# Kernel tuning notes

Measured on AMD Instinct MI355X. Metric: run time of the kernel, lower is better.

The kernel has to match this reference:

```python
import jax, jax.numpy as jnp
import numpy as np

HIDDEN, N_HEADS, N_KV, HEAD_DIM, CACHE_LEN = 4096, 32, 8, 128, 4096
N_REP = N_HEADS // N_KV
BATCH = 32


def setup_inputs() -> dict:
    key = jax.random.key(0)
    ks = jax.random.split(key, 7)
    x = jax.random.normal(ks[0], (BATCH, 1, HIDDEN), jnp.float32)
    k_cache = jax.random.normal(ks[1], (BATCH, N_KV, CACHE_LEN, HEAD_DIM), jnp.float32)
    v_cache = jax.random.normal(ks[2], (BATCH, N_KV, CACHE_LEN, HEAD_DIM), jnp.float32)
    s = 1.0 / np.sqrt(HIDDEN)
    wq = jax.random.normal(ks[3], (HIDDEN, N_HEADS * HEAD_DIM), jnp.float32) * s
    wk = jax.random.normal(ks[4], (HIDDEN, N_KV * HEAD_DIM), jnp.float32) * s
    wv = jax.random.normal(ks[5], (HIDDEN, N_KV * HEAD_DIM), jnp.float32) * s
    wo = jax.random.normal(ks[6], (N_HEADS * HEAD_DIM, HIDDEN), jnp.float32) * s
    return {"x": x, "k_cache": k_cache, "v_cache": v_cache,
            "wq": wq, "wk": wk, "wv": wv, "wo": wo}


def reference(x, k_cache, v_cache, wq, wk, wv, wo):
    b = x.shape[0]
    xt = x[:, 0, :]  # (b, hidden) -- single decode token
    # Projections; group query heads by kv head: (b, n_kv, n_rep, d)
    q = (xt @ wq).reshape(b, N_KV, N_REP, HEAD_DIM)
    k_new = (xt @ wk).reshape(b, N_KV, HEAD_DIM)
    v_new = (xt @ wv).reshape(b, N_KV, HEAD_DIM)
    scale = 1.0 / np.sqrt(HEAD_DIM).astype(np.float32)
    # GQA attention over cache: scores (b, n_kv, n_rep, cache_len)
    cache_scores = jnp.einsum('bknd,bksd->bkns', q, k_cache) * scale
    cache_probs = jax.nn.softmax(cache_scores, axis=-1)
    cache_out = jnp.einsum('bkns,bksd->bknd', cache_probs, v_cache)
    # New-token term: softmax over a length-1 axis is identically 1,
    # so the separate-pass attention over the new K/V reduces to v_new
    # broadcast over the n_rep query heads (keeps wk/wv in the graph via v_new).
    new_out = jnp.broadcast_to(v_new[:, :, None, :], cache_out.shape)
    out = (cache_out + new_out).reshape(b, 1, N_HEADS * HEAD_DIM)
    return out @ wo
```

## Files before the change

### kernel.cpp

```cpp
#include <hip/hip_runtime.h>
#include <hip/hip_bf16.h>

#define HIDDEN   4096
#define N_HEADS  32
#define N_KV     8
#define N_REP    4
#define HEAD_DIM 128
#define CACHE    4096
#define BATCH    32

#define PJ_THREADS 128
#define PJ_COLS    256
#define PJ_HCHUNK  128

typedef float f4v __attribute__((ext_vector_type(4)));

__global__ __launch_bounds__(128) void proj_kernel(
    const float* __restrict__ X,
    const float* __restrict__ W1, int ld1, int ncol1,
    const float* __restrict__ W2, int ld2,
    float* __restrict__ part, int ncols)
{
    __shared__ float xs[32 * PJ_HCHUNK];
    const int hc   = blockIdx.y;
    const int h0   = hc * PJ_HCHUNK;
    const int col0 = blockIdx.x * PJ_COLS;
    const int tid  = threadIdx.x;

    for (int i = tid * 4; i < 32 * PJ_HCHUNK; i += PJ_THREADS * 4) {
        int b = i >> 7, j = i & 127;
        *(float4*)&xs[i] = *(const float4*)&X[(size_t)b * HIDDEN + h0 + j];
    }
    __syncthreads();

    const int col = col0 + tid * 2;
    const float* Wp;
    size_t ld;
    if (col < ncol1) { Wp = W1 + (size_t)h0 * ld1 + col;           ld = ld1; }
    else             { Wp = W2 + (size_t)h0 * ld2 + (col - ncol1); ld = ld2; }

    float2 acc[32];
#pragma unroll
    for (int b = 0; b < 32; ++b) acc[b] = make_float2(0.f, 0.f);

    float2 wc[8], wn[8];
#pragma unroll
    for (int r = 0; r < 8; ++r) wc[r] = *(const float2*)(Wp + r * ld);
    Wp += 8 * ld;

#define PJ_COMPUTE(XR)                                                  \
    _Pragma("unroll")                                                   \
    for (int b = 0; b < 32; ++b) {                                      \
        float4 x0 = *(const float4*)((XR) + b * PJ_HCHUNK);             \
        float4 x1 = *(const float4*)((XR) + b * PJ_HCHUNK + 4);         \
        acc[b].x = fmaf(x0.x, wc[0].x, acc[b].x);                       \
        acc[b].y = fmaf(x0.x, wc[0].y, acc[b].y);                       \
        acc[b].x = fmaf(x0.y, wc[1].x, acc[b].x);                       \
        acc[b].y = fmaf(x0.y, wc[1].y, acc[b].y);                       \
        acc[b].x = fmaf(x0.z, wc[2].x, acc[b].x);                       \
        acc[b].y = fmaf(x0.z, wc[2].y, acc[b].y);                       \
        acc[b].x = fmaf(x0.w, wc[3].x, acc[b].x);                       \
        acc[b].y = fmaf(x0.w, wc[3].y, acc[b].y);                       \
        acc[b].x = fmaf(x1.x, wc[4].x, acc[b].x);                       \
        acc[b].y = fmaf(x1.x, wc[4].y, acc[b].y);                       \
        acc[b].x = fmaf(x1.y, wc[5].x, acc[b].x);                       \
        acc[b].y = fmaf(x1.y, wc[5].y, acc[b].y);                       \
        acc[b].x = fmaf(x1.z, wc[6].x, acc[b].x);                       \
        acc[b].y = fmaf(x1.z, wc[6].y, acc[b].y);                       \
        acc[b].x = fmaf(x1.w, wc[7].x, acc[b].x);                       \
        acc[b].y = fmaf(x1.w, wc[7].y, acc[b].y);                       \
    }

    for (int bt = 0; bt < (PJ_HCHUNK / 8) - 1; ++bt) {
#pragma unroll
        for (int r = 0; r < 8; ++r) wn[r] = *(const float2*)(Wp + r * ld);
        const float* xr = xs + bt * 8;
        PJ_COMPUTE(xr)
#pragma unroll
        for (int r = 0; r < 8; ++r) wc[r] = wn[r];
        Wp += 8 * ld;
    }
    {
        const float* xr = xs + PJ_HCHUNK - 8;
        PJ_COMPUTE(xr)
    }
#undef PJ_COMPUTE

    float* dst = part + ((size_t)hc * 32) * ncols + col;
#pragma unroll
    for (int b = 0; b < 32; ++b)
        *(float2*)(dst + (size_t)b * ncols) = acc[b];
}

__global__ __launch_bounds__(256) void combine_proj(
    const float* __restrict__ part, int ncols,
    float* __restrict__ dst1, int ld1, int ncol1,
    float* __restrict__ dst2, int ld2)
{
    const int col = blockIdx.x * 256 + threadIdx.x;
    const int b   = blockIdx.y;
    float s = 0.f;
#pragma unroll
    for (int i = 0; i < 32; ++i) s += part[((size_t)i * 32 + b) * ncols + col];
    if (col < ncol1) dst1[(size_t)b * ld1 + col] = s;
    else             dst2[(size_t)b * ld2 + (col - ncol1)] = s;
}


template<int CTRL>
__device__ __forceinline__ float dpp_ror(float x) {
    return __int_as_float(__builtin_amdgcn_update_dpp(
        0, __float_as_int(x), CTRL, 0xF, 0xF, true));
}

#define DOT8(PART, QA, QB)                         \
    PART = QA.x * ka.x;                            \
    PART = fmaf(QA.y, ka.y, PART);                 \
    PART = fmaf(QA.z, ka.z, PART);                 \
    PART = fmaf(QA.w, ka.w, PART);                 \
    PART = fmaf(QB.x, kb4.x, PART);                \
    PART = fmaf(QB.y, kb4.y, PART);                \
    PART = fmaf(QB.z, kb4.z, PART);                \
    PART = fmaf(QB.w, kb4.w, PART);

#define RED4_DPP(CTRL)                             \
    part0 += dpp_ror<CTRL>(part0);                 \
    part1 += dpp_ror<CTRL>(part1);                 \
    part2 += dpp_ror<CTRL>(part2);                 \
    part3 += dpp_ror<CTRL>(part3);

#define PVROW(PR, OA, OB)                          \
    OA.x = fmaf(PR, va.x,  OA.x);                  \
    OA.y = fmaf(PR, va.y,  OA.y);                  \
    OA.z = fmaf(PR, va.z,  OA.z);                  \
    OA.w = fmaf(PR, va.w,  OA.w);                  \
    OB.x = fmaf(PR, vb4.x, OB.x);                  \
    OB.y = fmaf(PR, vb4.y, OB.y);                  \
    OB.z = fmaf(PR, vb4.z, OB.z);                  \
    OB.w = fmaf(PR, vb4.w, OB.w);

#define REDV(V, M)                                 \
    V.x += __shfl_xor(V.x, M, 64);                 \
    V.y += __shfl_xor(V.y, M, 64);                 \
    V.z += __shfl_xor(V.z, M, 64);                 \
    V.w += __shfl_xor(V.w, M, 64);

__global__ __launch_bounds__(256, 4) void attn_kernel(
    const float* __restrict__ q,
    const float* __restrict__ kc,
    const float* __restrict__ vc,
    float* __restrict__ po,
    float* __restrict__ pl)
{
    const int bid   = blockIdx.x;
    const int pair  = bid >> 3;
    const int sg    = bid & 7;
    const int tid   = threadIdx.x;
    const int w     = tid >> 6;
    const int lane  = tid & 63;
    const int g     = lane >> 4;
    const int l     = lane & 15;
    const int split = sg * 4 + w;
    const int b     = pair >> 3;
    const int kv    = pair & 7;

    const float SCL = 0.08838834764831845f * 1.4426950408889634f;
    const float* qb = q + (size_t)b * HIDDEN + kv * 512 + l * 8;
    f4v q0a = *(const f4v*)(qb);         f4v q0b = *(const f4v*)(qb + 4);
    f4v q1a = *(const f4v*)(qb + 128);   f4v q1b = *(const f4v*)(qb + 132);
    f4v q2a = *(const f4v*)(qb + 256);   f4v q2b = *(const f4v*)(qb + 260);
    f4v q3a = *(const f4v*)(qb + 384);   f4v q3b = *(const f4v*)(qb + 388);
    q0a *= SCL; q0b *= SCL; q1a *= SCL; q1b *= SCL;
    q2a *= SCL; q2b *= SCL; q3a *= SCL; q3b *= SCL;

    const size_t base = (size_t)(b * N_KV + kv) * CACHE * HEAD_DIM;
    const int s0 = split * 128 + g;
    const float* kp = kc + base + (size_t)s0 * HEAD_DIM + l * 8;
    const float* vp = vc + base + (size_t)s0 * HEAD_DIM + l * 8;

    f4v o0a = 0.f, o0b = 0.f, o1a = 0.f, o1b = 0.f;
    f4v o2a = 0.f, o2b = 0.f, o3a = 0.f, o3b = 0.f;
    f4v lacv = 0.f;

    f4v ka  = __builtin_nontemporal_load((const f4v*)kp);
    f4v kb4 = __builtin_nontemporal_load((const f4v*)(kp + 4));
    f4v va  = __builtin_nontemporal_load((const f4v*)vp);
    f4v vb4 = __builtin_nontemporal_load((const f4v*)(vp + 4));

    for (int it = 0; it < 32; ++it) {
        const int adv = (it < 31) ? 512 : 0;
        const float* kn = kp + adv;
        const float* vn = vp + adv;
        f4v kna = __builtin_nontemporal_load((const f4v*)kn);
        f4v knb = __builtin_nontemporal_load((const f4v*)(kn + 4));
        f4v vna = __builtin_nontemporal_load((const f4v*)vn);
        f4v vnb = __builtin_nontemporal_load((const f4v*)(vn + 4));

        float part0, part1, part2, part3;
        DOT8(part0, q0a, q0b)
        DOT8(part1, q1a, q1b)
        DOT8(part2, q2a, q2b)
        DOT8(part3, q3a, q3b)

        RED4_DPP(0x121)
        RED4_DPP(0x122)
        RED4_DPP(0x124)
        RED4_DPP(0x128)

        float pr0 = __builtin_amdgcn_exp2f(part0);
        float pr1 = __builtin_amdgcn_exp2f(part1);
        float pr2 = __builtin_amdgcn_exp2f(part2);
        float pr3 = __builtin_amdgcn_exp2f(part3);
        lacv.x += pr0; lacv.y += pr1; lacv.z += pr2; lacv.w += pr3;

        PVROW(pr0, o0a, o0b)
        PVROW(pr1, o1a, o1b)
        PVROW(pr2, o2a, o2b)
        PVROW(pr3, o3a, o3b)

        ka = kna; kb4 = knb;
        va = vna; vb4 = vnb;
        kp += 512; vp += 512;
    }

    REDV(o0a, 16) REDV(o0b, 16) REDV(o1a, 16) REDV(o1b, 16)
    REDV(o2a, 16) REDV(o2b, 16) REDV(o3a, 16) REDV(o3b, 16)
    REDV(lacv, 16)
    REDV(o0a, 32) REDV(o0b, 32) REDV(o1a, 32) REDV(o1b, 32)
    REDV(o2a, 32) REDV(o2b, 32) REDV(o3a, 32) REDV(o3b, 32)
    REDV(lacv, 32)

    f4v wa = (g & 2) ? ((g & 1) ? o3a : o2a) : ((g & 1) ? o1a : o0a);
    f4v wb = (g & 2) ? ((g & 1) ? o3b : o2b) : ((g & 1) ? o1b : o0b);
    float lsel = (g & 2) ? ((g & 1) ? lacv.w : lacv.z)
                         : ((g & 1) ? lacv.y : lacv.x);

    float* pod = po + ((((size_t)pair * 32 + split) * 4 + g) * 128) + l * 8;
    *(f4v*)pod       = wa;
    *(f4v*)(pod + 4) = wb;
    if (l == 0) pl[((size_t)pair * 32 + split) * 4 + g] = lsel;
}

__global__ __launch_bounds__(256) void combine_attn(
    const float* __restrict__ po, const float* __restrict__ pl,
    const float* __restrict__ vnew, float* __restrict__ attnc)
{
    const int t    = blockIdx.x * 256 + threadIdx.x;
    const int pair = t >> 9;
    const int rem  = t & 511;
    const int r    = rem >> 7;
    const int d    = rem & 127;
    const int b    = pair >> 3;
    const int kv   = pair & 7;

    float os = 0.f, ls = 0.f;
#pragma unroll 4
    for (int s = 0; s < 32; ++s) {
        os += po[(((size_t)pair * 32 + s) * 4 + r) * 128 + d];
        ls += pl[((size_t)pair * 32 + s) * 4 + r];
    }
    float val = os / ls + vnew[(size_t)b * (N_KV * HEAD_DIM) + kv * 128 + d];
    attnc[(size_t)b * HIDDEN + kv * 512 + r * 128 + d] = val;
}

extern "C" void kernel_launch(void* const* d_in, const int* in_sizes, int n_in,
                              void* d_out, int out_size, void* d_ws, size_t ws_size,
                              hipStream_t stream)
{
    const float* x   = (const float*)d_in[0];
    const float* kc  = (const float*)d_in[1];
    const float* vc  = (const float*)d_in[2];
    const float* wq  = (const float*)d_in[3];
    const float* wv  = (const float*)d_in[5];
    const float* wo  = (const float*)d_in[6];
    float* out = (float*)d_out;

    float* ws    = (float*)d_ws;
    float* q     = ws;
    float* vnew  = ws + 131072;
    float* attnc = ws + 163840;
    float* S     = ws + 294912;
    float* pA    = S;
    float* po    = S;
    float* pl    = S + 4194304;
    float* pC    = S;

    proj_kernel<<<dim3(20, 32), PJ_THREADS, 0, stream>>>(x, wq, 4096, 4096, wv, 1024, pA, 5120);
    combine_proj<<<dim3(20, 32), 256, 0, stream>>>(pA, 5120, q, 4096, 4096, vnew, 1024);

    attn_kernel<<<2048, 256, 0, stream>>>(q, kc, vc, po, pl);
    combine_attn<<<512, 256, 0, stream>>>(po, pl, vnew, attnc);

    proj_kernel<<<dim3(16, 32), PJ_THREADS, 0, stream>>>(attnc, wo, 4096, 4096, wo, 4096, pC, 4096);
    combine_proj<<<dim3(16, 32), 256, 0, stream>>>(pC, 4096, out, 4096, 4096, out, 4096);
}
```

Measured before the change: 293.5 us.

## Remap attention lanes to four dims per lane and raise occupancy

Each 64-lane wave now maps 32 lanes across one 128-wide row with 4 elements per lane, and the two half-waves process interleaved rows. Each iteration loads two rows per half-wave instead of software-prefetching the next iteration's 8-wide K/V slices. This cuts per-thread accumulator and Q registers so launch bounds can rise from 4 to 8 blocks per CU, giving more waves in flight to hide memory latency on the bandwidth-bound KV-cache stream. The cost is an extra cross-row shuffle per score, a larger DPP reduction batch, and the loss of explicit prefetching.

```diff
diff --git a/kernel.cpp b/kernel.cpp
--- a/kernel.cpp
+++ b/kernel.cpp
@@ -113,31 +113,21 @@
         0, __float_as_int(x), CTRL, 0xF, 0xF, true));
 }
 
-#define DOT8(PART, QA, QB)                         \
-    PART = QA.x * ka.x;                            \
-    PART = fmaf(QA.y, ka.y, PART);                 \
-    PART = fmaf(QA.z, ka.z, PART);                 \
-    PART = fmaf(QA.w, ka.w, PART);                 \
-    PART = fmaf(QB.x, kb4.x, PART);                \
-    PART = fmaf(QB.y, kb4.y, PART);                \
-    PART = fmaf(QB.z, kb4.z, PART);                \
-    PART = fmaf(QB.w, kb4.w, PART);
-
-#define RED4_DPP(CTRL)                             \
-    part0 += dpp_ror<CTRL>(part0);                 \
-    part1 += dpp_ror<CTRL>(part1);                 \
-    part2 += dpp_ror<CTRL>(part2);                 \
-    part3 += dpp_ror<CTRL>(part3);
-
-#define PVROW(PR, OA, OB)                          \
-    OA.x = fmaf(PR, va.x,  OA.x);                  \
-    OA.y = fmaf(PR, va.y,  OA.y);                  \
-    OA.z = fmaf(PR, va.z,  OA.z);                  \
-    OA.w = fmaf(PR, va.w,  OA.w);                  \
-    OB.x = fmaf(PR, vb4.x, OB.x);                  \
-    OB.y = fmaf(PR, vb4.y, OB.y);                  \
-    OB.z = fmaf(PR, vb4.z, OB.z);                  \
-    OB.w = fmaf(PR, vb4.w, OB.w);
+#define DOT4(S, Q, K)                              \
+    S = Q.x * K.x;                                 \
+    S = fmaf(Q.y, K.y, S);                         \
+    S = fmaf(Q.z, K.z, S);                         \
+    S = fmaf(Q.w, K.w, S);
+
+#define RED8_DPP(CTRL)                             \
+    sA0 += dpp_ror<CTRL>(sA0);                     \
+    sA1 += dpp_ror<CTRL>(sA1);                     \
+    sA2 += dpp_ror<CTRL>(sA2);                     \
+    sA3 += dpp_ror<CTRL>(sA3);                     \
+    sB0 += dpp_ror<CTRL>(sB0);                     \
+    sB1 += dpp_ror<CTRL>(sB1);                     \
+    sB2 += dpp_ror<CTRL>(sB2);                     \
+    sB3 += dpp_ror<CTRL>(sB3);
 
 #define REDV(V, M)                                 \
     V.x += __shfl_xor(V.x, M, 64);                 \
@@ -145,7 +135,7 @@
     V.z += __shfl_xor(V.z, M, 64);                 \
     V.w += __shfl_xor(V.w, M, 64);
 
-__global__ __launch_bounds__(256, 4) void attn_kernel(
+__global__ __launch_bounds__(256, 8) void attn_kernel(
     const float* __restrict__ q,
     const float* __restrict__ kc,
     const float* __restrict__ vc,
@@ -158,87 +148,96 @@
     const int tid   = threadIdx.x;
     const int w     = tid >> 6;
     const int lane  = tid & 63;
-    const int g     = lane >> 4;
-    const int l     = lane & 15;
+    const int h     = lane >> 5;
+    const int c     = lane & 31;
     const int split = sg * 4 + w;
     const int b     = pair >> 3;
     const int kv    = pair & 7;
 
     const float SCL = 0.08838834764831845f * 1.4426950408889634f;
-    const float* qb = q + (size_t)b * HIDDEN + kv * 512 + l * 8;
-    f4v q0a = *(const f4v*)(qb);         f4v q0b = *(const f4v*)(qb + 4);
-    f4v q1a = *(const f4v*)(qb + 128);   f4v q1b = *(const f4v*)(qb + 132);
-    f4v q2a = *(const f4v*)(qb + 256);   f4v q2b = *(const f4v*)(qb + 260);
-    f4v q3a = *(const f4v*)(qb + 384);   f4v q3b = *(const f4v*)(qb + 388);
-    q0a *= SCL; q0b *= SCL; q1a *= SCL; q1b *= SCL;
-    q2a *= SCL; q2b *= SCL; q3a *= SCL; q3b *= SCL;
+    const float* qbp = q + (size_t)b * HIDDEN + kv * 512 + c * 4;
+    f4v q0 = *(const f4v*)(qbp);
+    f4v q1 = *(const f4v*)(qbp + 128);
+    f4v q2 = *(const f4v*)(qbp + 256);
+    f4v q3 = *(const f4v*)(qbp + 384);
+    q0 *= SCL; q1 *= SCL; q2 *= SCL; q3 *= SCL;
 
     const size_t base = (size_t)(b * N_KV + kv) * CACHE * HEAD_DIM;
-    const int s0 = split * 128 + g;
-    const float* kp = kc + base + (size_t)s0 * HEAD_DIM + l * 8;
-    const float* vp = vc + base + (size_t)s0 * HEAD_DIM + l * 8;
-
-    f4v o0a = 0.f, o0b = 0.f, o1a = 0.f, o1b = 0.f;
-    f4v o2a = 0.f, o2b = 0.f, o3a = 0.f, o3b = 0.f;
+    const int j0 = split * 128;
+    const float* kp = kc + base + (size_t)(j0 + h) * HEAD_DIM + c * 4;
+    const float* vp = vc + base + (size_t)(j0 + h) * HEAD_DIM + c * 4;
+
+    f4v o0 = 0.f, o1 = 0.f, o2 = 0.f, o3 = 0.f;
     f4v lacv = 0.f;
 
-    f4v ka  = __builtin_nontemporal_load((const f4v*)kp);
-    f4v kb4 = __builtin_nontemporal_load((const f4v*)(kp + 4));
-    f4v va  = __builtin_nontemporal_load((const f4v*)vp);
-    f4v vb4 = __builtin_nontemporal_load((const f4v*)(vp + 4));
-
     for (int it = 0; it < 32; ++it) {
-        const int adv = (it < 31) ? 512 : 0;
-        const float* kn = kp + adv;
-        const float* vn = vp + adv;
-        f4v kna = __builtin_nontemporal_load((const f4v*)kn);
-        f4v knb = __builtin_nontemporal_load((const f4v*)(kn + 4));
-        f4v vna = __builtin_nontemporal_load((const f4v*)vn);
-        f4v vnb = __builtin_nontemporal_load((const f4v*)(vn + 4));
-
-        float part0, part1, part2, part3;
-        DOT8(part0, q0a, q0b)
-        DOT8(part1, q1a, q1b)
-        DOT8(part2, q2a, q2b)
-        DOT8(part3, q3a, q3b)
-
-        RED4_DPP(0x121)
-        RED4_DPP(0x122)
-        RED4_DPP(0x124)
-        RED4_DPP(0x128)
-
-        float pr0 = __builtin_amdgcn_exp2f(part0);
-        float pr1 = __builtin_amdgcn_exp2f(part1);
-        float pr2 = __builtin_amdgcn_exp2f(part2);
-        float pr3 = __builtin_amdgcn_exp2f(part3);
-        lacv.x += pr0; lacv.y += pr1; lacv.z += pr2; lacv.w += pr3;
-
-        PVROW(pr0, o0a, o0b)
-        PVROW(pr1, o1a, o1b)
-        PVROW(pr2, o2a, o2b)
-        PVROW(pr3, o3a, o3b)
-
-        ka = kna; kb4 = knb;
-        va = vna; vb4 = vnb;
+        f4v ka = __builtin_nontemporal_load((const f4v*)kp);
+        f4v kb = __builtin_nontemporal_load((const f4v*)(kp + 256));
+        f4v va = __builtin_nontemporal_load((const f4v*)vp);
+        f4v vb = __builtin_nontemporal_load((const f4v*)(vp + 256));
+
+        float sA0, sA1, sA2, sA3, sB0, sB1, sB2, sB3;
+        DOT4(sA0, q0, ka)  DOT4(sA1, q1, ka)
+        DOT4(sA2, q2, ka)  DOT4(sA3, q3, ka)
+        DOT4(sB0, q0, kb)  DOT4(sB1, q1, kb)
+        DOT4(sB2, q2, kb)  DOT4(sB3, q3, kb)
+
+        RED8_DPP(0x121)
+        RED8_DPP(0x122)
+        RED8_DPP(0x124)
+        RED8_DPP(0x128)
+        sA0 += __shfl_xor(sA0, 16, 64);
+        sA1 += __shfl_xor(sA1, 16, 64);
+        sA2 += __shfl_xor(sA2, 16, 64);
+        sA3 += __shfl_xor(sA3, 16, 64);
+        sB0 += __shfl_xor(sB0, 16, 64);
+        sB1 += __shfl_xor(sB1, 16, 64);
+        sB2 += __shfl_xor(sB2, 16, 64);
+        sB3 += __shfl_xor(sB3, 16, 64);
+
+        float pA0 = __builtin_amdgcn_exp2f(sA0);
+        float pA1 = __builtin_amdgcn_exp2f(sA1);
+        float pA2 = __builtin_amdgcn_exp2f(sA2);
+        float pA3 = __builtin_amdgcn_exp2f(sA3);
+        float pB0 = __builtin_amdgcn_exp2f(sB0);
+        float pB1 = __builtin_amdgcn_exp2f(sB1);
+        float pB2 = __builtin_amdgcn_exp2f(sB2);
+        float pB3 = __builtin_amdgcn_exp2f(sB3);
+
+        lacv.x += pA0 + pB0;
+        lacv.y += pA1 + pB1;
+        lacv.z += pA2 + pB2;
+        lacv.w += pA3 + pB3;
+
+        o0.x = fmaf(pA0, va.x, o0.x); o0.x = fmaf(pB0, vb.x, o0.x);
+        o0.y = fmaf(pA0, va.y, o0.y); o0.y = fmaf(pB0, vb.y, o0.y);
+        o0.z = fmaf(pA0, va.z, o0.z); o0.z = fmaf(pB0, vb.z, o0.z);
+        o0.w = fmaf(pA0, va.w, o0.w); o0.w = fmaf(pB0, vb.w, o0.w);
+        o1.x = fmaf(pA1, va.x, o1.x); o1.x = fmaf(pB1, vb.x, o1.x);
+        o1.y = fmaf(pA1, va.y, o1.y); o1.y = fmaf(pB1, vb.y, o1.y);
+        o1.z = fmaf(pA1, va.z, o1.z); o1.z = fmaf(pB1, vb.z, o1.z);
+        o1.w = fmaf(pA1, va.w, o1.w); o1.w = fmaf(pB1, vb.w, o1.w);
+        o2.x = fmaf(pA2, va.x, o2.x); o2.x = fmaf(pB2, vb.x, o2.x);
+        o2.y = fmaf(pA2, va.y, o2.y); o2.y = fmaf(pB2, vb.y, o2.y);
+        o2.z = fmaf(pA2, va.z, o2.z); o2.z = fmaf(pB2, vb.z, o2.z);
+        o2.w = fmaf(pA2, va.w, o2.w); o2.w = fmaf(pB2, vb.w, o2.w);
+        o3.x = fmaf(pA3, va.x, o3.x); o3.x = fmaf(pB3, vb.x, o3.x);
+        o3.y = fmaf(pA3, va.y, o3.y); o3.y = fmaf(pB3, vb.y, o3.y);
+        o3.z = fmaf(pA3, va.z, o3.z); o3.z = fmaf(pB3, vb.z, o3.z);
+        o3.w = fmaf(pA3, va.w, o3.w); o3.w = fmaf(pB3, vb.w, o3.w);
+
         kp += 512; vp += 512;
     }
 
-    REDV(o0a, 16) REDV(o0b, 16) REDV(o1a, 16) REDV(o1b, 16)
-    REDV(o2a, 16) REDV(o2b, 16) REDV(o3a, 16) REDV(o3b, 16)
-    REDV(lacv, 16)
-    REDV(o0a, 32) REDV(o0b, 32) REDV(o1a, 32) REDV(o1b, 32)
-    REDV(o2a, 32) REDV(o2b, 32) REDV(o3a, 32) REDV(o3b, 32)
-    REDV(lacv, 32)
-
-    f4v wa = (g & 2) ? ((g & 1) ? o3a : o2a) : ((g & 1) ? o1a : o0a);
-    f4v wb = (g & 2) ? ((g & 1) ? o3b : o2b) : ((g & 1) ? o1b : o0b);
-    float lsel = (g & 2) ? ((g & 1) ? lacv.w : lacv.z)
-                         : ((g & 1) ? lacv.y : lacv.x);
-
-    float* pod = po + ((((size_t)pair * 32 + split) * 4 + g) * 128) + l * 8;
-    *(f4v*)pod       = wa;
-    *(f4v*)(pod + 4) = wb;
-    if (l == 0) pl[((size_t)pair * 32 + split) * 4 + g] = lsel;
+    REDV(o0, 32) REDV(o1, 32) REDV(o2, 32) REDV(o3, 32) REDV(lacv, 32)
+
+    f4v w0 = h ? o2 : o0;
+    f4v w1 = h ? o3 : o1;
+    float* pod = po + (((size_t)pair * 32 + split) * 4 + 2 * h) * 128 + c * 4;
+    *(f4v*)pod         = w0;
+    *(f4v*)(pod + 128) = w1;
+    if (lane == 0)
+        *(f4v*)(pl + ((size_t)pair * 32 + split) * 4) = lacv;
 }
 
 __global__ __launch_bounds__(256) void combine_attn(
```

New measurement: 259.9 us. 11.5% less time.
